# Optimization experiments

Measured on AMD Instinct MI355X. Metric: run time of the kernel, lower is better.

## Reference

```python
import jax, jax.numpy as jnp
import numpy as np

B, C, H, W = 32, 256, 64, 64
MH = 8
E = 524288
TEMPERATURE = 0.1
LN_EPS = 1e-5


def setup_inputs() -> dict:
    key = jax.random.key(0)
    ks = jax.random.split(key, 6)
    n_nodes = B * H * W
    scale = 1.0 / np.sqrt(C).astype(np.float32)
    img = jax.random.normal(ks[0], (B, C, H, W), jnp.float32)
    all_edge = jax.random.randint(ks[1], (2, E), 0, n_nodes, dtype=jnp.int64)
    Wp = jax.random.normal(ks[2], (C, C), jnp.float32) * scale
    bp = jnp.zeros((C,), jnp.float32)
    Wg = jax.random.normal(ks[3], (C, C), jnp.float32) * scale
    bg = jnp.zeros((C,), jnp.float32)
    ln_gamma = jnp.ones((C,), jnp.float32)
    ln_beta = jnp.zeros((C,), jnp.float32)
    diff_query = jax.random.normal(ks[4], (1, 1, C), jnp.float32) * scale  # xavier-ish
    return {"img": img, "all_edge": all_edge, "Wp": Wp, "bp": bp,
            "Wg": Wg, "bg": bg, "ln_gamma": ln_gamma, "ln_beta": ln_beta,
            "diff_query": diff_query, "mask_head": MH}


def _gcn_conv(x, row, col, Wg, bg, num_nodes):
    # PyG GCNConv with add_self_loops=True, symmetric normalization.
    loop = jnp.arange(num_nodes, dtype=row.dtype)
    row = jnp.concatenate([row, loop])
    col = jnp.concatenate([col, loop])
    deg = jnp.zeros((num_nodes,), x.dtype).at[col].add(1.0)
    dinv = jnp.where(deg > 0, jax.lax.rsqrt(deg), 0.0)
    norm = dinv[row] * dinv[col]                      # [E+N]
    xl = x @ Wg                                       # [N, C]
    msg = xl[row] * norm[:, None]                     # gather + scale
    agg = jax.ops.segment_sum(msg, col, num_segments=num_nodes)
    return agg + bg


def reference(img, all_edge, Wp, bp, Wg, bg, ln_gamma, ln_beta, diff_query, mask_head):
    b, c, h, w = img.shape
    node_num = h * w
    num_nodes = b * node_num
    hd = c // mask_head
    # [B,C,H,W] -> [B, N, C]
    x = jnp.transpose(img, (0, 2, 3, 1)).reshape(b, node_num, c)
    x = x @ Wp + bp
    x = x.reshape(num_nodes, c)
    g = _gcn_conv(x, all_edge[0], all_edge[1], Wg, bg, num_nodes)
    g = jax.nn.gelu(g, approximate=False)             # nn.GELU (exact)
    g = g + x
    mu = jnp.mean(g, axis=-1, keepdims=True)
    var = jnp.mean(jnp.square(g - mu), axis=-1, keepdims=True)
    img_graph = (g - mu) * jax.lax.rsqrt(var + LN_EPS) * ln_gamma + ln_beta
    # multi-head adjacency: query [B*MH, 1, hd], keys [B*MH, N, hd]
    q = jnp.broadcast_to(diff_query, (b, 1, c)).reshape(b * mask_head, 1, hd)
    k = img_graph.reshape(b, node_num, mask_head, hd)
    k = jnp.transpose(k, (0, 2, 1, 3)).reshape(b * mask_head, node_num, hd)
    adj = jnp.einsum('bod,bnd->bon', q, k) / TEMPERATURE
    adj = jax.nn.softmax(adj, axis=-1)
    return img_graph, adj
```

## Files before the change

kernel.cpp:

```cpp
#include <hip/hip_runtime.h>

typedef unsigned short u16;
typedef __attribute__((ext_vector_type(8))) short short8;
typedef __attribute__((ext_vector_type(4))) float f32x4;
typedef __attribute__((ext_vector_type(16))) float f32x16;

#define AS1C(p) ((const __attribute__((address_space(1))) void*)(p))
#define AS3(p)  ((__attribute__((address_space(3))) void*)(p))

constexpr int CC    = 256;
constexpr int HWSZ  = 4096;
constexpr int NNODE = 131072;
constexpr int EEDG  = 524288;
constexpr int CAP   = 32;

__device__ __forceinline__ float bf2f(u16 h){ unsigned u = ((unsigned)h)<<16; float f; __builtin_memcpy(&f,&u,4); return f; }
__device__ __forceinline__ u16 f2bf(float f){ unsigned u; __builtin_memcpy(&u,&f,4); return (u16)((u + 0x7FFFu + ((u>>16)&1u))>>16); }

__device__ __forceinline__ float gelu_fast(float v){
  float y = 0.7978845608f*(v + 0.044715f*v*v*v);
  float e = __expf(2.0f*y);
  float r = __builtin_amdgcn_rcpf(e + 1.0f);
  return 0.5f*v*(2.0f - 2.0f*r) + 0.0f*v;
}

__device__ __forceinline__ void unpack8(uint4 q, float f[8]){
  unsigned w0=q.x,w1=q.y,w2=q.z,w3=q.w;
  unsigned l0=w0<<16, h0=w0&0xffff0000u, l1=w1<<16, h1=w1&0xffff0000u;
  unsigned l2=w2<<16, h2=w2&0xffff0000u, l3=w3<<16, h3=w3&0xffff0000u;
  __builtin_memcpy(&f[0],&l0,4); __builtin_memcpy(&f[1],&h0,4);
  __builtin_memcpy(&f[2],&l1,4); __builtin_memcpy(&f[3],&h1,4);
  __builtin_memcpy(&f[4],&l2,4); __builtin_memcpy(&f[5],&h2,4);
  __builtin_memcpy(&f[6],&l3,4); __builtin_memcpy(&f[7],&h3,4);
}

__global__ __launch_bounds__(256) void transpose_split(const float* __restrict__ src,
                                                       u16* __restrict__ dhi, u16* __restrict__ dlo,
                                                       int R, int Ccols, size_t sb_in, size_t sb_out)
{
  __shared__ float t[64][65];
  const float* s = src + blockIdx.z*sb_in + (size_t)(blockIdx.y*64)*Ccols + blockIdx.x*64;
  size_t obase   = blockIdx.z*sb_out + (size_t)(blockIdx.x*64)*R + blockIdx.y*64;
  int tid = threadIdx.x;
  for (int i=0;i<4;++i){
    int idx = i*256 + tid;
    int r = idx>>4, q = idx&15;
    float4 v = *(const float4*)(s + (size_t)r*Ccols + q*4);
    t[r][q*4+0]=v.x; t[r][q*4+1]=v.y; t[r][q*4+2]=v.z; t[r][q*4+3]=v.w;
  }
  __syncthreads();
  for (int i=0;i<2;++i){
    int idx = i*256 + tid;
    int rr = idx>>3, ch = idx&7;
    u16 hi[8], lo[8];
    for (int j=0;j<8;++j){
      float f = t[ch*8+j][rr];
      u16 h = f2bf(f); hi[j] = h;
      lo[j] = f2bf(f - bf2f(h));
    }
    *(uint4*)(dhi + obase + (size_t)rr*R + ch*8) = *(uint4*)hi;
    if (dlo) *(uint4*)(dlo + obase + (size_t)rr*R + ch*8) = *(uint4*)lo;
  }
}

__global__ __launch_bounds__(256,2) void gemm_img(const float* __restrict__ img,
                                                  const u16* __restrict__ Bt,
                                                  const float* __restrict__ bias,
                                                  u16* __restrict__ C)
{
  __shared__ float Afp[2][32*64];
  __shared__ u16   Bs[2][256*32];
  const int tid = threadIdx.x, wid = tid>>6, lane = tid&63;
  const int row0 = blockIdx.x*64;
  const int bb = row0 >> 12, hw0 = row0 & 4095;
  const float* abase = img + (size_t)bb*CC*HWSZ + hw0;
  const int l31 = lane&31, lh = lane>>5;

  f32x16 acc[2][2];
  #pragma unroll
  for (int i=0;i<2;++i)
    #pragma unroll
    for (int j=0;j<2;++j)
      #pragma unroll
      for (int e=0;e<16;++e) acc[i][j][e]=0.f;

#define STAGE_IMG(buf, kt)                                                             \
  {                                                                                    \
    _Pragma("unroll")                                                                  \
    for (int it=0; it<2; ++it){                                                        \
      int qb = (it*4+wid)*64;                                                          \
      int q  = qb + lane;                                                              \
      int c  = q>>4, mq = q&15;                                                        \
      __builtin_amdgcn_global_load_lds(AS1C(abase + (size_t)((kt)+c)*HWSZ + mq*4),     \
                                       AS3(&Afp[buf][qb*4]), 16, 0, 0);                \
    }                                                                                  \
    _Pragma("unroll")                                                                  \
    for (int it=0; it<4; ++it){                                                        \
      int qb = (it*4+wid)*64;                                                          \
      int q  = qb + lane;                                                              \
      int m  = q>>2, sc = q&3;                                                         \
      int gs = sc ^ ((m>>1)&3);                                                        \
      __builtin_amdgcn_global_load_lds(AS1C(Bt + (size_t)m*256 + (kt) + gs*8),         \
                                       AS3(&Bs[buf][qb*8]), 16, 0, 0);                 \
    }                                                                                  \
  }

  STAGE_IMG(0, 0)
  asm volatile("s_waitcnt vmcnt(0)" ::: "memory");
  __syncthreads();

  for (int t=0; t<8; ++t) {
    int cur = t&1;
    if (t<7) STAGE_IMG(cur^1, (t+1)*32)

    short8 ah[2][2], bfr[2][2];
    #pragma unroll
    for (int fm=0; fm<2; ++fm)
      #pragma unroll
      for (int kh=0; kh<2; ++kh) {
        int r  = fm*32 + l31;
        int cb = kh*16 + lh*8;
        unsigned w[4];
        #pragma unroll
        for (int p=0; p<4; ++p) {
          unsigned u0, u1;
          float f0 = Afp[cur][(cb+2*p  )*64 + r];
          float f1 = Afp[cur][(cb+2*p+1)*64 + r];
          __builtin_memcpy(&u0,&f0,4); __builtin_memcpy(&u1,&f1,4);
          w[p] = __builtin_amdgcn_perm(u1, u0, 0x07060302u);
        }
        __builtin_memcpy(&ah[fm][kh], w, 16);
      }
    #pragma unroll
    for (int fn=0; fn<2; ++fn)
      #pragma unroll
      for (int kh=0; kh<2; ++kh) {
        int col = wid*64 + fn*32 + l31;
        int sb  = (kh*2 + lh) ^ ((col>>1)&3);
        bfr[fn][kh] = *(const short8*)&Bs[cur][col*32 + sb*8];
      }
    #pragma unroll
    for (int kh=0; kh<2; ++kh)
      #pragma unroll
      for (int fm=0; fm<2; ++fm)
        #pragma unroll
        for (int fn=0; fn<2; ++fn)
          acc[fm][fn] = __builtin_amdgcn_mfma_f32_32x32x16_bf16(ah[fm][kh], bfr[fn][kh], acc[fm][fn], 0, 0, 0);
    asm volatile("s_waitcnt vmcnt(0)" ::: "memory");
    __syncthreads();
  }
#undef STAGE_IMG

  #pragma unroll
  for (int fn=0; fn<2; ++fn) {
    int col = wid*64 + fn*32 + l31;
    float bv = bias ? bias[col] : 0.f;
    #pragma unroll
    for (int fm=0; fm<2; ++fm) {
      int rbase = row0 + fm*32 + 4*lh;
      #pragma unroll
      for (int reg=0; reg<16; ++reg) {
        int row = rbase + (reg&3) + 8*(reg>>2);
        C[(size_t)row*256 + col] = f2bf(acc[fm][fn][reg] + bv);
      }
    }
  }
}

__global__ __launch_bounds__(256,2) void gemm1p(const u16* __restrict__ A,
                                                const u16* __restrict__ Bt,
                                                u16* __restrict__ C)
{
  __shared__ u16 As[2][64*32];
  __shared__ u16 Bs[2][256*32];
  const int tid = threadIdx.x, wid = tid>>6, lane = tid&63;
  const int row0 = blockIdx.x*64;
  const int l31 = lane&31, lh = lane>>5;

  f32x16 acc[2][2];
  #pragma unroll
  for (int i=0;i<2;++i)
    #pragma unroll
    for (int j=0;j<2;++j)
      #pragma unroll
      for (int e=0;e<16;++e) acc[i][j][e]=0.f;

#define STAGE_AB(buf, kt)                                                              \
  {                                                                                    \
    {                                                                                  \
      int qb = wid*64;                                                                 \
      int q  = qb + lane;                                                              \
      int m  = q>>2, sc = q&3;                                                         \
      int gs = sc ^ ((m>>1)&3);                                                        \
      __builtin_amdgcn_global_load_lds(AS1C(A + (size_t)(row0+m)*256 + (kt) + gs*8),   \
                                       AS3(&As[buf][qb*8]), 16, 0, 0);                 \
    }                                                                                  \
    _Pragma("unroll")                                                                  \
    for (int it=0; it<4; ++it){                                                        \
      int qb = (it*4+wid)*64;                                                          \
      int q  = qb + lane;                                                              \
      int m  = q>>2, sc = q&3;                                                         \
      int gs = sc ^ ((m>>1)&3);                                                        \
      __builtin_amdgcn_global_load_lds(AS1C(Bt + (size_t)m*256 + (kt) + gs*8),         \
                                       AS3(&Bs[buf][qb*8]), 16, 0, 0);                 \
    }                                                                                  \
  }

  STAGE_AB(0, 0)
  asm volatile("s_waitcnt vmcnt(0)" ::: "memory");
  __syncthreads();

  for (int t=0; t<8; ++t) {
    int cur = t&1;
    if (t<7) STAGE_AB(cur^1, (t+1)*32)

    short8 af[2][2], bfr[2][2];
    #pragma unroll
    for (int fm=0; fm<2; ++fm)
      #pragma unroll
      for (int kh=0; kh<2; ++kh) {
        int row = fm*32 + l31;
        int sa  = (kh*2 + lh) ^ ((row>>1)&3);
        af[fm][kh] = *(const short8*)&As[cur][row*32 + sa*8];
      }
    #pragma unroll
    for (int fn=0; fn<2; ++fn)
      #pragma unroll
      for (int kh=0; kh<2; ++kh) {
        int col = wid*64 + fn*32 + l31;
        int sb  = (kh*2 + lh) ^ ((col>>1)&3);
        bfr[fn][kh] = *(const short8*)&Bs[cur][col*32 + sb*8];
      }
    #pragma unroll
    for (int kh=0; kh<2; ++kh)
      #pragma unroll
      for (int fm=0; fm<2; ++fm)
        #pragma unroll
        for (int fn=0; fn<2; ++fn)
          acc[fm][fn] = __builtin_amdgcn_mfma_f32_32x32x16_bf16(af[fm][kh], bfr[fn][kh], acc[fm][fn], 0, 0, 0);
    asm volatile("s_waitcnt vmcnt(0)" ::: "memory");
    __syncthreads();
  }
#undef STAGE_AB

  #pragma unroll
  for (int fn=0; fn<2; ++fn) {
    int col = wid*64 + fn*32 + l31;
    #pragma unroll
    for (int fm=0; fm<2; ++fm) {
      int rbase = row0 + fm*32 + 4*lh;
      #pragma unroll
      for (int reg=0; reg<16; ++reg) {
        int row = rbase + (reg&3) + 8*(reg>>2);
        C[(size_t)row*256 + col] = f2bf(acc[fm][fn][reg]);
      }
    }
  }
}

__global__ void fill_all(const int* __restrict__ row, const int* __restrict__ col,
                         int* __restrict__ cur, int* __restrict__ bucket){
  int e = blockIdx.x*256 + threadIdx.x;
  if (e >= EEDG) return;
  int c = col[e];
  int s = atomicAdd(&cur[c], 1);
  if (s < CAP) bucket[(size_t)c*CAP + s] = row[e];
}
__global__ void calc_dinv(const int* __restrict__ cnt, float* __restrict__ dinv){
  int n = blockIdx.x*256 + threadIdx.x;
  if (n < NNODE) dinv[n] = rsqrtf((float)cnt[n] + 1.0f);
}

__global__ __launch_bounds__(256) void fused_agg(
    const u16* __restrict__ xl, const u16* __restrict__ xhi,
    const int* __restrict__ cnt, const float* __restrict__ dinv, const int* __restrict__ bucket,
    const float* __restrict__ bgv, const float* __restrict__ gam, const float* __restrict__ bet,
    const float* __restrict__ qv, float* __restrict__ outg, float* __restrict__ logits)
{
  const int wid = threadIdx.x>>6, lane = threadIdx.x&63;
  const int half = lane>>5, sl = lane&31;
  const int n = blockIdx.x*8 + wid*2 + half;
  const int c0 = sl*8;
  const float dn = dinv[n];
  int lim = cnt[n]; if (lim > CAP) lim = CAP;

  int rl = bucket[(size_t)n*CAP + sl];
  if (sl >= lim) rl = n;
  float wl = (sl < lim) ? dinv[rl]*dn : 0.0f;

  uint4 qh = *(const uint4*)(xhi + (size_t)n*256 + c0);

  float a[8];
  {
    uint4 q = *(const uint4*)(xl + (size_t)n*256 + c0);
    unpack8(q, a);
    float wself = dn*dn;
    #pragma unroll
    for (int j=0;j<8;++j) a[j] *= wself;
  }

  int limR = (lim + 3) & ~3;
  for (int s=0; s<limR; s+=4) {
    int b0 = half*32 + s;
    int  r0 = __shfl(rl, b0),   r1 = __shfl(rl, b0+1);
    int  r2 = __shfl(rl, b0+2), r3 = __shfl(rl, b0+3);
    float w0 = __shfl(wl, b0),   w1 = __shfl(wl, b0+1);
    float w2 = __shfl(wl, b0+2), w3 = __shfl(wl, b0+3);
    uint4 q0 = *(const uint4*)(xl + (size_t)r0*256 + c0);
    uint4 q1 = *(const uint4*)(xl + (size_t)r1*256 + c0);
    uint4 q2 = *(const uint4*)(xl + (size_t)r2*256 + c0);
    uint4 q3 = *(const uint4*)(xl + (size_t)r3*256 + c0);
    float f0[8], f1[8], f2[8], f3[8];
    unpack8(q0, f0); unpack8(q1, f1); unpack8(q2, f2); unpack8(q3, f3);
    #pragma unroll
    for (int j=0;j<8;++j) a[j] += f0[j]*w0 + f1[j]*w1 + f2[j]*w2 + f3[j]*w3;
  }

  float xv[8];
  unpack8(qh, xv);

  float4 b0v = *(const float4*)(bgv + c0), b1v = *(const float4*)(bgv + c0 + 4);
  float bgs[8] = {b0v.x,b0v.y,b0v.z,b0v.w,b1v.x,b1v.y,b1v.z,b1v.w};
  float g[8];
  float s1 = 0.f, s2 = 0.f;
  #pragma unroll
  for (int j=0;j<8;++j){
    g[j] = gelu_fast(a[j] + bgs[j]) + xv[j];
    s1 += g[j]; s2 += g[j]*g[j];
  }
  #pragma unroll
  for (int off=16; off; off>>=1){ s1 += __shfl_xor(s1, off); s2 += __shfl_xor(s2, off); }
  float mu  = s1*(1.0f/256.0f);
  float var = s2*(1.0f/256.0f) - mu*mu;
  float inv = rsqrtf(var + 1e-5f);

  float4 g0 = *(const float4*)(gam + c0), g1 = *(const float4*)(gam + c0 + 4);
  float4 e0 = *(const float4*)(bet + c0), e1 = *(const float4*)(bet + c0 + 4);
  float gms[8] = {g0.x,g0.y,g0.z,g0.w,g1.x,g1.y,g1.z,g1.w};
  float bts[8] = {e0.x,e0.y,e0.z,e0.w,e1.x,e1.y,e1.z,e1.w};
  float y[8];
  #pragma unroll
  for (int j=0;j<8;++j) y[j] = (g[j]-mu)*inv*gms[j] + bts[j];

  float4 o0 = {y[0],y[1],y[2],y[3]}, o1 = {y[4],y[5],y[6],y[7]};
  *reinterpret_cast<float4*>(outg + (size_t)n*256 + c0)     = o0;
  *reinterpret_cast<float4*>(outg + (size_t)n*256 + c0 + 4) = o1;

  float4 q0 = *(const float4*)(qv + c0), q1 = *(const float4*)(qv + c0 + 4);
  float qs[8] = {q0.x,q0.y,q0.z,q0.w,q1.x,q1.y,q1.z,q1.w};
  float dq = 0.f;
  #pragma unroll
  for (int j=0;j<8;++j) dq += y[j]*qs[j];
  dq += __shfl_xor(dq,1); dq += __shfl_xor(dq,2);
  if ((sl&3)==0){
    int b = n>>12, p = n&4095, h = sl>>2;
    logits[(size_t)(b*8+h)*4096 + p] = dq*10.0f;
  }
}

__global__ __launch_bounds__(256) void softmax_rows(const float* __restrict__ logits, float* __restrict__ outa){
  int r = blockIdx.x;
  const float* p = logits + (size_t)r*4096;
  int tid = threadIdx.x;
  int wid = tid>>6, lane = tid&63;
  __shared__ float redm[4];
  __shared__ float reds[4];
  float v[16];
  float mx = -1e30f;
  for (int i=0;i<16;++i){ v[i] = p[tid + i*256]; mx = fmaxf(mx, v[i]); }
  for (int off=32; off; off>>=1) mx = fmaxf(mx, __shfl_xor(mx, off));
  if (lane==0) redm[wid]=mx;
  __syncthreads();
  mx = fmaxf(fmaxf(redm[0],redm[1]), fmaxf(redm[2],redm[3]));
  float sum = 0.f;
  for (int i=0;i<16;++i){ v[i] = expf(v[i]-mx); sum += v[i]; }
  for (int off=32; off; off>>=1) sum += __shfl_xor(sum, off);
  if (lane==0) reds[wid]=sum;
  __syncthreads();
  sum = reds[0]+reds[1]+reds[2]+reds[3];
  float rinv = 1.0f/sum;
  for (int i=0;i<16;++i) outa[(size_t)r*4096 + tid + i*256] = v[i]*rinv;
}

extern "C" void kernel_launch(void* const* d_in, const int* in_sizes, int n_in,
                              void* d_out, int out_size, void* d_ws, size_t ws_size,
                              hipStream_t stream)
{
  const float* img  = (const float*)d_in[0];
  const int* edges  = (const int*)d_in[1];
  const float* Wp   = (const float*)d_in[2];
  const float* bp   = (const float*)d_in[3];
  const float* Wg   = (const float*)d_in[4];
  const float* bg   = (const float*)d_in[5];
  const float* lng  = (const float*)d_in[6];
  const float* lnb  = (const float*)d_in[7];
  const float* dq   = (const float*)d_in[8];
  char* ws = (char*)d_ws;

  constexpr size_t REG  = (size_t)NNODE*CC*2;
  constexpr size_t WTS  = 2u*131072;
  constexpr size_t GBLK = 524288u*2 + (size_t)NNODE*CAP*4 + (size_t)256*4096*4;
  if (ws_size < 2*REG + WTS + GBLK) return;

  u16* x_hi = (u16*)(ws + 0);
  u16* xl   = (u16*)(ws + REG);
  char* wts  = ws + 2*REG;
  char* gblk = wts + WTS;

  u16* WpT_hi = (u16*)(wts);
  u16* WgT_hi = (u16*)(wts + 131072);
  int*   cur    = (int*)(gblk);
  float* dinv   = (float*)(gblk + 524288);
  int*   bucket = (int*)(gblk + 1048576);
  float* logits = (float*)(gblk + 1048576 + (size_t)NNODE*CAP*4);

  transpose_split<<<dim3(4,4,1), 256, 0, stream>>>(Wp, WpT_hi, nullptr, 256, 256, 0, 0);
  transpose_split<<<dim3(4,4,1), 256, 0, stream>>>(Wg, WgT_hi, nullptr, 256, 256, 0, 0);

  hipMemsetAsync(cur, 0, 524288, stream);
  fill_all <<<2048, 256, 0, stream>>>(edges, edges+EEDG, cur, bucket);
  calc_dinv<<<512,  256, 0, stream>>>(cur, dinv);

  gemm_img<<<2048, 256, 0, stream>>>(img, WpT_hi, bp, x_hi);
  gemm1p<<<2048, 256, 0, stream>>>(x_hi, WgT_hi, xl);

  float* outg = (float*)d_out;
  float* outa = (float*)d_out + (size_t)NNODE*CC;
  fused_agg<<<NNODE/8, 256, 0, stream>>>(xl, x_hi, cur, dinv, bucket,
                                         bg, lng, lnb, dq, outg, logits);
  softmax_rows<<<256, 256, 0, stream>>>(logits, outa);
}
```

Measured before the change: 233.3 us.

## Convert img tile to bf16 in registers before LDS staging in first GEMM

The first GEMM no longer stages the fp32 image tile into LDS via direct global-to-LDS loads. Each thread now loads float2 pairs into registers, packs them to bf16 and writes a swizzled bf16 A tile after the MFMA block. This halves the A-tile LDS footprint and replaces per-fragment scalar LDS reads plus perm ops with single vector reads. Launch bounds are raised to 3 blocks per SU on both GEMMs to lift occupancy, at the cost of register pressure and of global loads now passing through VGPRs.

Measured after the change: 228.8 us. Within noise of the previous version (-1.9%).

```diff
diff --git a/kernel.cpp b/kernel.cpp
--- a/kernel.cpp
+++ b/kernel.cpp
@@ -1,8 +1,8 @@
 #include <hip/hip_runtime.h>
+#include <hip/hip_bf16.h>
 
 typedef unsigned short u16;
 typedef __attribute__((ext_vector_type(8))) short short8;
-typedef __attribute__((ext_vector_type(4))) float f32x4;
 typedef __attribute__((ext_vector_type(16))) float f32x16;
 
 #define AS1C(p) ((const __attribute__((address_space(1))) void*)(p))
@@ -17,11 +17,17 @@
 __device__ __forceinline__ float bf2f(u16 h){ unsigned u = ((unsigned)h)<<16; float f; __builtin_memcpy(&f,&u,4); return f; }
 __device__ __forceinline__ u16 f2bf(float f){ unsigned u; __builtin_memcpy(&u,&f,4); return (u16)((u + 0x7FFFu + ((u>>16)&1u))>>16); }
 
+__device__ __forceinline__ unsigned pkbf(float a, float b){
+  float2 t; t.x = a; t.y = b;
+  __hip_bfloat162 h = __float22bfloat162_rn(t);
+  unsigned u; __builtin_memcpy(&u,&h,4); return u;
+}
+
 __device__ __forceinline__ float gelu_fast(float v){
   float y = 0.7978845608f*(v + 0.044715f*v*v*v);
   float e = __expf(2.0f*y);
   float r = __builtin_amdgcn_rcpf(e + 1.0f);
-  return 0.5f*v*(2.0f - 2.0f*r) + 0.0f*v;
+  return 0.5f*v*(2.0f - 2.0f*r);
 }
 
 __device__ __forceinline__ void unpack8(uint4 q, float f[8]){
@@ -63,18 +69,23 @@
   }
 }
 
-__global__ __launch_bounds__(256,2) void gemm_img(const float* __restrict__ img,
-                                                  const u16* __restrict__ Bt,
-                                                  const float* __restrict__ bias,
-                                                  u16* __restrict__ C)
+__global__ __launch_bounds__(256,3) void gemm_t1(const float* __restrict__ img,
+                                                 const u16* __restrict__ Bt,
+                                                 const float* __restrict__ bias,
+                                                 u16* __restrict__ C)
 {
-  __shared__ float Afp[2][32*64];
-  __shared__ u16   Bs[2][256*32];
+  __shared__ u16 As[2][64*32];
+  __shared__ u16 Bs[2][256*32];
   const int tid = threadIdx.x, wid = tid>>6, lane = tid&63;
   const int row0 = blockIdx.x*64;
-  const int bb = row0 >> 12, hw0 = row0 & 4095;
+  const int bb = row0>>12, hw0 = row0&4095;
   const float* abase = img + (size_t)bb*CC*HWSZ + hw0;
   const int l31 = lane&31, lh = lane>>5;
+  const int mpr = l31;
+  const int cb  = wid*8 + lh*4;
+  const int cs  = wid ^ (mpr&3);
+  const int wa0 = (2*mpr  )*32 + cs*8 + lh*4;
+  const int wa1 = (2*mpr+1)*32 + cs*8 + lh*4;
 
   f32x16 acc[2][2];
   #pragma unroll
@@ -84,52 +95,48 @@
       #pragma unroll
       for (int e=0;e<16;++e) acc[i][j][e]=0.f;
 
-#define STAGE_IMG(buf, kt)                                                             \
-  {                                                                                    \
-    _Pragma("unroll")                                                                  \
-    for (int it=0; it<2; ++it){                                                        \
-      int qb = (it*4+wid)*64;                                                          \
-      int q  = qb + lane;                                                              \
-      int c  = q>>4, mq = q&15;                                                        \
-      __builtin_amdgcn_global_load_lds(AS1C(abase + (size_t)((kt)+c)*HWSZ + mq*4),     \
-                                       AS3(&Afp[buf][qb*4]), 16, 0, 0);                \
-    }                                                                                  \
-    _Pragma("unroll")                                                                  \
+  float2 ar[4];
+
+#define LOADA(kt)                                                                      \
+  { _Pragma("unroll")                                                                  \
+    for (int i=0;i<4;++i)                                                              \
+      ar[i] = *(const float2*)(abase + (size_t)((kt)+cb+i)*HWSZ + 2*mpr); }
+
+#define WRITEA(buf)                                                                    \
+  { uint2 p0, p1;                                                                      \
+    p0.x = pkbf(ar[0].x, ar[1].x); p0.y = pkbf(ar[2].x, ar[3].x);                      \
+    p1.x = pkbf(ar[0].y, ar[1].y); p1.y = pkbf(ar[2].y, ar[3].y);                      \
+    *(uint2*)&As[buf][wa0] = p0;                                                       \
+    *(uint2*)&As[buf][wa1] = p1; }
+
+#define STAGE_B(buf, kt)                                                               \
+  { _Pragma("unroll")                                                                  \
     for (int it=0; it<4; ++it){                                                        \
       int qb = (it*4+wid)*64;                                                          \
       int q  = qb + lane;                                                              \
       int m  = q>>2, sc = q&3;                                                         \
       int gs = sc ^ ((m>>1)&3);                                                        \
       __builtin_amdgcn_global_load_lds(AS1C(Bt + (size_t)m*256 + (kt) + gs*8),         \
-                                       AS3(&Bs[buf][qb*8]), 16, 0, 0);                 \
-    }                                                                                  \
-  }
-
-  STAGE_IMG(0, 0)
+                                       AS3(&Bs[buf][qb*8]), 16, 0, 0); } }
+
+  LOADA(0)
+  STAGE_B(0, 0)
+  WRITEA(0)
   asm volatile("s_waitcnt vmcnt(0)" ::: "memory");
   __syncthreads();
 
   for (int t=0; t<8; ++t) {
     int cur = t&1;
-    if (t<7) STAGE_IMG(cur^1, (t+1)*32)
-
-    short8 ah[2][2], bfr[2][2];
+    if (t<7) { LOADA((t+1)*32) STAGE_B(cur^1, (t+1)*32) }
+
+    short8 af[2][2], bfr[2][2];
     #pragma unroll
     for (int fm=0; fm<2; ++fm)
       #pragma unroll
       for (int kh=0; kh<2; ++kh) {
-        int r  = fm*32 + l31;
-        int cb = kh*16 + lh*8;
-        unsigned w[4];
-        #pragma unroll
-        for (int p=0; p<4; ++p) {
-          unsigned u0, u1;
-          float f0 = Afp[cur][(cb+2*p  )*64 + r];
-          float f1 = Afp[cur][(cb+2*p+1)*64 + r];
-          __builtin_memcpy(&u0,&f0,4); __builtin_memcpy(&u1,&f1,4);
-          w[p] = __builtin_amdgcn_perm(u1, u0, 0x07060302u);
-        }
-        __builtin_memcpy(&ah[fm][kh], w, 16);
+        int row = fm*32 + l31;
+        int sa  = (kh*2 + lh) ^ ((row>>1)&3);
+        af[fm][kh] = *(const short8*)&As[cur][row*32 + sa*8];
       }
     #pragma unroll
     for (int fn=0; fn<2; ++fn)
@@ -145,11 +152,15 @@
       for (int fm=0; fm<2; ++fm)
         #pragma unroll
         for (int fn=0; fn<2; ++fn)
-          acc[fm][fn] = __builtin_amdgcn_mfma_f32_32x32x16_bf16(ah[fm][kh], bfr[fn][kh], acc[fm][fn], 0, 0, 0);
+          acc[fm][fn] = __builtin_amdgcn_mfma_f32_32x32x16_bf16(af[fm][kh], bfr[fn][kh], acc[fm][fn], 0, 0, 0);
+
+    if (t<7) WRITEA(cur^1)
     asm volatile("s_waitcnt vmcnt(0)" ::: "memory");
     __syncthreads();
   }
-#undef STAGE_IMG
+#undef STAGE_B
+#undef WRITEA
+#undef LOADA
 
   #pragma unroll
   for (int fn=0; fn<2; ++fn) {
@@ -167,8 +178,9 @@
   }
 }
 
-__global__ __launch_bounds__(256,2) void gemm1p(const u16* __restrict__ A,
+__global__ __launch_bounds__(256,3) void gemm1p(const u16* __restrict__ A,
                                                 const u16* __restrict__ Bt,
+                                                const float* __restrict__ bias,
                                                 u16* __restrict__ C)
 {
   __shared__ u16 As[2][64*32];
@@ -246,13 +258,14 @@
   #pragma unroll
   for (int fn=0; fn<2; ++fn) {
     int col = wid*64 + fn*32 + l31;
+    float bv = bias ? bias[col] : 0.f;
     #pragma unroll
     for (int fm=0; fm<2; ++fm) {
       int rbase = row0 + fm*32 + 4*lh;
       #pragma unroll
       for (int reg=0; reg<16; ++reg) {
         int row = rbase + (reg&3) + 8*(reg>>2);
-        C[(size_t)row*256 + col] = f2bf(acc[fm][fn][reg]);
+        C[(size_t)row*256 + col] = f2bf(acc[fm][fn][reg] + bv);
       }
     }
   }
@@ -402,8 +415,8 @@
   constexpr size_t GBLK = 524288u*2 + (size_t)NNODE*CAP*4 + (size_t)256*4096*4;
   if (ws_size < 2*REG + WTS + GBLK) return;
 
-  u16* x_hi = (u16*)(ws + 0);
-  u16* xl   = (u16*)(ws + REG);
+  u16* buf0 = (u16*)(ws + 0);
+  u16* buf1 = (u16*)(ws + REG);
   char* wts  = ws + 2*REG;
   char* gblk = wts + WTS;
 
@@ -421,12 +434,12 @@
   fill_all <<<2048, 256, 0, stream>>>(edges, edges+EEDG, cur, bucket);
   calc_dinv<<<512,  256, 0, stream>>>(cur, dinv);
 
-  gemm_img<<<2048, 256, 0, stream>>>(img, WpT_hi, bp, x_hi);
-  gemm1p<<<2048, 256, 0, stream>>>(x_hi, WgT_hi, xl);
+  gemm_t1<<<2048, 256, 0, stream>>>(img, WpT_hi, bp, buf0);
+  gemm1p<<<2048, 256, 0, stream>>>(buf0, WgT_hi, nullptr, buf1);
 
   float* outg = (float*)d_out;
   float* outa = (float*)d_out + (size_t)NNODE*CC;
-  fused_agg<<<NNODE/8, 256, 0, stream>>>(xl, x_hi, cur, dinv, bucket,
+  fused_agg<<<NNODE/8, 256, 0, stream>>>(buf1, buf0, cur, dinv, bucket,
                                          bg, lng, lnb, dq, outg, logits);
   softmax_rows<<<256, 256, 0, stream>>>(logits, outa);
 }
```
